# Optimization experiments

Measured on AMD Instinct MI355X. Metric: run time of the kernel, lower is better.

The kernel has to match this reference:

```python
import jax, jax.numpy as jnp
import numpy as np

HID = 64      # hidden_dim
HEADS = 4     # attention heads
CH = HID // HEADS  # 16 per-head channels
EDIM = 6      # edge_dim
NEG = 0.2     # leaky_relu negative slope


def _glorot(key, shape):
    fan_in, fan_out = shape[0], shape[-1]
    s = np.sqrt(6.0 / (fan_in + fan_out)).astype(np.float32)
    return jax.random.uniform(key, shape, jnp.float32, -s, s)


def setup_inputs() -> dict:
    key = jax.random.key(0)
    ks = iter(jax.random.split(key, 48))
    N, E, T = 100000, 1200000, 20000
    inp = {
        "x": jax.random.normal(next(ks), (N, 7), jnp.float32),
        "pos": jax.random.normal(next(ks), (N, 3), jnp.float32),
        "node_type": jax.random.randint(next(ks), (N,), 0, 2),
        "edge_index": jax.random.randint(next(ks), (2, E), 0, N),
        "edge_attr": jax.random.normal(next(ks), (E, EDIM), jnp.float32),
        "num_tracks": T,
        "hidden_state": jax.random.normal(next(ks), (T, HID), jnp.float32),
        # params
        "type_emb": jax.random.normal(next(ks), (2, 8), jnp.float32),
        "enc_W1": _glorot(next(ks), (18, HID)), "enc_b1": jnp.zeros((HID,), jnp.float32),
        "enc_W2": _glorot(next(ks), (HID, HID)), "enc_b2": jnp.zeros((HID,), jnp.float32),
        "gru_Wi": _glorot(next(ks), (HID, 3 * HID)), "gru_bi": jnp.zeros((3 * HID,), jnp.float32),
        "gru_Wh": _glorot(next(ks), (HID, 3 * HID)), "gru_bh": jnp.zeros((3 * HID,), jnp.float32),
        "dec_W1": _glorot(next(ks), (HID, HID)), "dec_b1": jnp.zeros((HID,), jnp.float32),
        "dec_W2": _glorot(next(ks), (HID, 7)), "dec_b2": jnp.zeros((7,), jnp.float32),
    }
    for g in ("g1", "g2"):
        inp[g + "_Wl"] = _glorot(next(ks), (HID, HID))
        inp[g + "_bl"] = jnp.zeros((HID,), jnp.float32)
        inp[g + "_Wr"] = _glorot(next(ks), (HID, HID))
        inp[g + "_br"] = jnp.zeros((HID,), jnp.float32)
        inp[g + "_We"] = _glorot(next(ks), (EDIM, HID))
        inp[g + "_att"] = _glorot(next(ks), (HEADS, CH))
        inp[g + "_bias"] = jnp.zeros((HID,), jnp.float32)
    return inp


def _segment_softmax(e, seg, n):
    m = jax.ops.segment_max(e, seg, num_segments=n)
    m = jnp.where(jnp.isfinite(m), m, 0.0)
    ex = jnp.exp(e - m[seg])
    s = jax.ops.segment_sum(ex, seg, num_segments=n)
    return ex / (s[seg] + 1e-16)


def _gatv2(h, src, dst, eattr, Wl, bl, Wr, br, We, att, bias):
    N = h.shape[0]
    xl = (h @ Wl + bl).reshape(N, HEADS, CH)
    xr = (h @ Wr + br).reshape(N, HEADS, CH)
    ea = (eattr @ We).reshape(-1, HEADS, CH)
    g = jax.nn.leaky_relu(xl[src] + xr[dst] + ea, NEG)      # [E, H, C]
    e = jnp.einsum('ehc,hc->eh', g, att)                     # [E, H]
    alpha = _segment_softmax(e, dst, N)                      # [E, H]
    msg = xl[src] * alpha[..., None]                         # [E, H, C]
    out = jax.ops.segment_sum(msg, dst, num_segments=N)
    return out.reshape(N, HID) + bias, alpha


def reference(x, pos, node_type, edge_index, edge_attr, num_tracks, hidden_state,
              type_emb, enc_W1, enc_b1, enc_W2, enc_b2,
              g1_Wl, g1_bl, g1_Wr, g1_br, g1_We, g1_att, g1_bias,
              g2_Wl, g2_bl, g2_Wr, g2_br, g2_We, g2_att, g2_bias,
              gru_Wi, gru_bi, gru_Wh, gru_bh,
              dec_W1, dec_b1, dec_W2, dec_b2):
    N = x.shape[0]
    h = jnp.concatenate([x, pos, type_emb[node_type]], axis=-1)
    h = jax.nn.relu(h @ enc_W1 + enc_b1) @ enc_W2 + enc_b2

    # PyG GATv2Conv: add self loops, edge_attr fill_value='mean' (mean of incoming edges)
    src, dst = edge_index[0], edge_index[1]
    deg = jax.ops.segment_sum(jnp.ones(src.shape[0], jnp.float32), dst, num_segments=N)
    loop_attr = jax.ops.segment_sum(edge_attr, dst, num_segments=N) / jnp.maximum(deg, 1.0)[:, None]
    ar = jnp.arange(N)
    src_a = jnp.concatenate([src, ar])
    dst_a = jnp.concatenate([dst, ar])
    eattr_a = jnp.concatenate([edge_attr, loop_attr], axis=0)

    h1, a1 = _gatv2(h, src_a, dst_a, eattr_a, g1_Wl, g1_bl, g1_Wr, g1_br, g1_We, g1_att, g1_bias)
    h1 = jax.nn.relu(h1)
    h2, a2 = _gatv2(h1, src_a, dst_a, eattr_a, g2_Wl, g2_bl, g2_Wr, g2_br, g2_We, g2_att, g2_bias)

    # GRUCell on the first num_tracks nodes
    ht = h2[:num_tracks]
    gi = ht @ gru_Wi + gru_bi
    gh = hidden_state @ gru_Wh + gru_bh
    r = jax.nn.sigmoid(gi[:, :HID] + gh[:, :HID])
    z = jax.nn.sigmoid(gi[:, HID:2 * HID] + gh[:, HID:2 * HID])
    n = jnp.tanh(gi[:, 2 * HID:] + r * gh[:, 2 * HID:])
    new_tracks = (1.0 - z) * n + z * hidden_state

    new_full = jnp.concatenate([new_tracks, h2[num_tracks:]], axis=0)
    out = jax.nn.relu(new_full @ dec_W1 + dec_b1) @ dec_W2 + dec_b2  # [N, 7]
    final = out.at[:, :3].set(pos + out[:, :3])
    final = final.at[:, 3:6].set(x[:, :3] + out[:, 3:6])
    return final, new_full, a1, a2
```

## Files before the change

kernel.cpp:

```cpp
#include <hip/hip_runtime.h>

#define NEG 0.2f
#define SCHUNK 1024
typedef unsigned short u16;

__device__ __forceinline__ float sigmoidf_(float v){ return 1.f/(1.f+__expf(-v)); }
__device__ __forceinline__ int rfl_(int v){ return __builtin_amdgcn_readfirstlane(v); }
__device__ __forceinline__ float bf2f_(u16 u){ return __uint_as_float(((unsigned)u)<<16); }
__device__ __forceinline__ u16 f2bf_(float f){
  unsigned u = __float_as_uint(f);
  u += 0x7FFFu + ((u>>16)&1u);
  return (u16)(u>>16);
}
template<int C>
__device__ __forceinline__ float dppadd_(float p){
  int r = __builtin_amdgcn_update_dpp(0, __float_as_int(p), C, 0xF, 0xF, true);
  return p + __int_as_float(r);
}
__device__ __forceinline__ float dppsum16_(float p){
  p = dppadd_<0x121>(p);
  p = dppadd_<0x122>(p);
  p = dppadd_<0x124>(p);
  p = dppadd_<0x128>(p);
  return p;
}

__global__ __launch_bounds__(256) void enc_kernel(
    const float* __restrict__ x, const float* __restrict__ pos,
    const int* __restrict__ ntype, const float* __restrict__ temb,
    const float* __restrict__ W1, const float* __restrict__ b1,
    const float* __restrict__ W2, const float* __restrict__ b2,
    float* __restrict__ hout, int N)
{
  __shared__ float sW1[18*64];
  __shared__ float sW2[4096];
  __shared__ float fT[4][8*20];
  __shared__ float tT[4][8*64];
  for (int i=threadIdx.x; i<18*64; i+=256) sW1[i]=W1[i];
  for (int i=threadIdx.x; i<4096; i+=256)  sW2[i]=W2[i];
  __syncthreads();
  int lane = threadIdx.x & 63;
  int wid  = threadIdx.x >> 6;
  int n0 = (blockIdx.x*4 + wid)*8;
  if (n0 >= N) return;
  float b1v=b1[lane], b2v=b2[lane];
  #pragma unroll
  for (int m=0;m<8;m++){
    int n=n0+m; float fv=0.f;
    if (n<N){
      if (lane<7)       fv=x[(size_t)n*7+lane];
      else if (lane<10) fv=pos[(size_t)n*3+lane-7];
      else if (lane<18) fv=temb[ntype[n]*8+lane-10];
    }
    if (lane<20) fT[wid][m*20+lane]=fv;
  }
  float t[8];
  #pragma unroll
  for (int m=0;m<8;m++) t[m]=b1v;
  #pragma unroll 2
  for (int k=0;k<18;k++){
    float w=sW1[k*64+lane];
    #pragma unroll
    for (int m=0;m<8;m++) t[m] += fT[wid][m*20+k]*w;
  }
  #pragma unroll
  for (int m=0;m<8;m++){ t[m]=fmaxf(t[m],0.f); tT[wid][m*64+lane]=t[m]; }
  float o[8];
  #pragma unroll
  for (int m=0;m<8;m++) o[m]=b2v;
  #pragma unroll 2
  for (int k=0;k<64;k++){
    float w=sW2[k*64+lane];
    #pragma unroll
    for (int m=0;m<8;m++) o[m] += tT[wid][m*64+k]*w;
  }
  #pragma unroll
  for (int m=0;m<8;m++){ int n=n0+m; if (n<N) hout[(size_t)n*64+lane]=o[m]; }
}

__global__ void deg_kernel(const int* __restrict__ ei, int* __restrict__ deg, int E)
{
  int e = blockIdx.x*256 + threadIdx.x;
  if (e>=E) return;
  atomicAdd(deg + ei[E+e], 1);
}

__global__ __launch_bounds__(256) void scan_reduce(const int* __restrict__ deg, int* __restrict__ bsum, int N)
{
  int base = blockIdx.x*SCHUNK + threadIdx.x*4;
  int s=0;
  #pragma unroll
  for (int j=0;j<4;j++){ int i=base+j; s += (i<N)? deg[i]+1 : 0; }
  #pragma unroll
  for (int d=1;d<64;d<<=1) s += __shfl_xor(s,d);
  __shared__ int ws[4];
  if ((threadIdx.x&63)==0) ws[threadIdx.x>>6]=s;
  __syncthreads();
  if (threadIdx.x==0) bsum[blockIdx.x]=ws[0]+ws[1]+ws[2]+ws[3];
}

__global__ __launch_bounds__(1024) void scan_bsums(const int* __restrict__ bsum, int* __restrict__ bscan, int NB)
{
  int tid = threadIdx.x;
  int lane = tid&63, w = tid>>6;
  int v = (tid<NB)? bsum[tid] : 0;
  int inc = v;
  #pragma unroll
  for (int d=1;d<64;d<<=1){ int t=__shfl_up(inc,d); if (lane>=d) inc+=t; }
  __shared__ int wsum[16], woff[16];
  if (lane==63) wsum[w]=inc;
  __syncthreads();
  if (w==0){
    int s=(lane<16)?wsum[lane]:0; int sc=s;
    #pragma unroll
    for (int d=1;d<16;d<<=1){ int t=__shfl_up(sc,d); if (lane>=d) sc+=t; }
    if (lane<16) woff[lane]=sc-s;
  }
  __syncthreads();
  int excl = woff[w] + inc - v;
  if (tid<NB) bscan[tid]=excl;
}

__global__ __launch_bounds__(256) void scan_final(const int* __restrict__ deg, const int* __restrict__ bscan,
                                                  int* __restrict__ offs, int N)
{
  int lane = threadIdx.x&63, w = threadIdx.x>>6;
  int base = blockIdx.x*SCHUNK + threadIdx.x*4;
  int v[4]; int s=0;
  #pragma unroll
  for (int j=0;j<4;j++){ int i=base+j; v[j]=(i<N)?deg[i]+1:0; s+=v[j]; }
  int inc=s;
  #pragma unroll
  for (int d=1;d<64;d<<=1){ int t=__shfl_up(inc,d); if (lane>=d) inc+=t; }
  __shared__ int wsum[4], woff[4];
  if (lane==63) wsum[w]=inc;
  __syncthreads();
  if (threadIdx.x==0){ woff[0]=0; woff[1]=wsum[0]; woff[2]=wsum[0]+wsum[1]; woff[3]=wsum[0]+wsum[1]+wsum[2]; }
  __syncthreads();
  int excl = bscan[blockIdx.x] + woff[w] + (inc - s);
  #pragma unroll
  for (int j=0;j<4;j++){ int i=base+j; if (i<N) offs[i]=excl; excl+=v[j]; }
}

__global__ void fill_kernel(const int* __restrict__ ei, const int* __restrict__ offs,
                            int* __restrict__ cursor, int2* __restrict__ csr2, int E)
{
  int e = blockIdx.x*256 + threadIdx.x;
  if (e >= E) return;
  int dst = ei[E + e];
  int p = atomicAdd(cursor + dst, 1);
  csr2[offs[dst] + p] = make_int2(e, ei[e]);
}

__global__ __launch_bounds__(256) void xfrm_kernel(
    const float* __restrict__ hin,
    const float* __restrict__ Wl, const float* __restrict__ bl,
    const float* __restrict__ Wr, const float* __restrict__ br,
    u16* __restrict__ xlo, u16* __restrict__ xro, int N)
{
  __shared__ float sWl[4096], sWr[4096];
  __shared__ float hT[4][16*64];
  for (int i=threadIdx.x;i<4096;i+=256){ sWl[i]=Wl[i]; sWr[i]=Wr[i]; }
  __syncthreads();
  int lane=threadIdx.x&63;
  int wid=threadIdx.x>>6;
  int n0=(blockIdx.x*4+wid)*16;
  if (n0>=N) return;
  #pragma unroll
  for (int m=0;m<16;m++){
    int n=n0+m;
    hT[wid][m*64+lane] = (n<N)? hin[(size_t)n*64+lane] : 0.f;
  }
  float blv=bl[lane], brv=br[lane];
  float al[16], ar[16];
  #pragma unroll
  for (int m=0;m<16;m++){ al[m]=blv; ar[m]=brv; }
  #pragma unroll 2
  for (int k=0;k<64;k++){
    float wl=sWl[k*64+lane], wr=sWr[k*64+lane];
    #pragma unroll
    for (int m=0;m<16;m++){
      float hb = hT[wid][m*64+k];
      al[m]+=hb*wl; ar[m]+=hb*wr;
    }
  }
  #pragma unroll
  for (int m=0;m<16;m++){
    int n=n0+m;
    if (n<N){ xlo[(size_t)n*64+lane]=f2bf_(al[m]); xro[(size_t)n*64+lane]=f2bf_(ar[m]); }
  }
}

#define EDGE_STEP(EIDX, EADD, XV) do {                                       \
    float s_ = (XV) + xrv + (EADD);                                          \
    s_ = fmaxf(s_, NEG*s_);                                                  \
    float p_ = dppsum16_(s_*attv);                                           \
    if (isbase) aout[(size_t)(EIDX)*4+h] = p_;                               \
    if (__all(p_ <= mmax)) {                                                 \
      float w_ = __expf(p_ - mmax);                                          \
      ssum += w_; acc += w_*(XV);                                            \
    } else {                                                                 \
      float mn_ = fmaxf(mmax, p_);                                           \
      float sc_ = __expf(mmax - mn_);                                        \
      float w_  = __expf(p_ - mn_);                                          \
      ssum = ssum*sc_ + w_;                                                  \
      acc  = acc*sc_ + w_*(XV);                                              \
      mmax = mn_;                                                            \
    }                                                                        \
  } while(0)

#define EDGE_PRE(J) \
    int e##J = rfl_(c##J.x), s##J = rfl_(c##J.y); \
    const float2* q##J = (const float2*)(eattr + (size_t)e##J*6); \
    float2 A##J=q##J[0], B##J=q##J[1], C##J=q##J[2]; \
    float xv##J = bf2f_(xlb[(size_t)s##J*64+lane]);

#define EDGE_BODY(J) \
    float d##J = A##J.x*we0 + A##J.y*we1 + B##J.x*we2 + B##J.y*we3 + C##J.x*we4 + C##J.y*we5; \
    dsum += d##J; \
    EDGE_STEP(e##J, d##J, xv##J);

__global__ __launch_bounds__(256) void gat_kernel(
    const int2* __restrict__ csr2, const int* __restrict__ offs, const int* __restrict__ deg,
    const float* __restrict__ eattr,
    const u16* __restrict__ xlb, const u16* __restrict__ xrb,
    const float* __restrict__ We, const float* __restrict__ att,
    const float* __restrict__ bias,
    float* __restrict__ aout, float2* __restrict__ msbuf,
    float* __restrict__ hout,
    int E, int N, int do_relu)
{
  int lane = threadIdx.x & 63;
  int n = blockIdx.x*4 + (threadIdx.x>>6);
  if (n >= N) return;
  float we0=We[lane], we1=We[64+lane], we2=We[128+lane],
        we3=We[192+lane], we4=We[256+lane], we5=We[320+lane];
  float attv = att[lane];
  float bv = bias[lane];
  float xrv = bf2f_(xrb[(size_t)n*64+lane]);
  int h = lane >> 4;
  bool isbase = (lane & 15) == 0;
  int o0 = rfl_(offs[n]);
  int dg = rfl_(deg[n]);
  int oend = o0 + dg;
  float mmax = -3.402823e38f, ssum=0.f, acc=0.f, dsum=0.f;
  int o = o0;
  for (; o+4 <= oend; o += 4){
    int2 c0=csr2[o], c1=csr2[o+1], c2=csr2[o+2], c3=csr2[o+3];
    EDGE_PRE(0); EDGE_PRE(1); EDGE_PRE(2); EDGE_PRE(3);
    EDGE_BODY(0); EDGE_BODY(1); EDGE_BODY(2); EDGE_BODY(3);
  }
  for (; o < oend; ++o){
    int2 c0=csr2[o];
    EDGE_PRE(0);
    EDGE_BODY(0);
  }
  {
    float dS = dsum * (1.f/fmaxf((float)dg,1.f));
    float xvS = bf2f_(xlb[(size_t)n*64+lane]);
    EDGE_STEP(E+n, dS, xvS);
  }
  float sinv = 1.f/(ssum + 1e-16f);
  if (isbase) msbuf[(size_t)n*4+h] = make_float2(mmax, sinv);
  float outv = acc*sinv + bv;
  if (do_relu) outv = fmaxf(outv, 0.f);
  hout[(size_t)n*64+lane] = outv;
}

__global__ void alpha_kernel(const int* __restrict__ ei, const float2* __restrict__ msbuf,
                             float4* __restrict__ aout4, int E, int N)
{
  int e = blockIdx.x*256 + threadIdx.x;
  if (e >= E+N) return;
  int dst = (e<E)? ei[E+e] : (e-E);
  float4 r = aout4[e];
  const float2* mp = msbuf + (size_t)dst*4;
  float2 m0=mp[0], m1=mp[1], m2=mp[2], m3=mp[3];
  float4 o;
  o.x = __expf(r.x - m0.x)*m0.y;
  o.y = __expf(r.y - m1.x)*m1.y;
  o.z = __expf(r.z - m2.x)*m2.y;
  o.w = __expf(r.w - m3.x)*m3.y;
  aout4[e] = o;
}

__global__ __launch_bounds__(256) void grudec_kernel(
    const float* __restrict__ h2, const float* __restrict__ hid,
    const float* __restrict__ Wi, const float* __restrict__ bi,
    const float* __restrict__ Wh, const float* __restrict__ bh,
    const int* __restrict__ Tptr,
    const float* __restrict__ W1, const float* __restrict__ b1,
    const float* __restrict__ W2, const float* __restrict__ b2,
    const float* __restrict__ x, const float* __restrict__ pos,
    float* __restrict__ nf, float* __restrict__ fout, int N)
{
  __shared__ float sW1[4096];
  __shared__ float sW2[448];
  __shared__ float sb2[7];
  __shared__ float tT[4][8*64];
  __shared__ float pT[4][8*64];
  for (int i=threadIdx.x;i<4096;i+=256) sW1[i]=W1[i];
  for (int i=threadIdx.x;i<448;i+=256) sW2[i]=W2[i];
  if (threadIdx.x<7)  sb2[threadIdx.x]=b2[threadIdx.x];
  __syncthreads();
  int lane = threadIdx.x & 63;
  int wid  = threadIdx.x >> 6;
  int n0 = (blockIdx.x*4 + wid)*8;
  if (n0 >= N) return;
  int T = *Tptr;
  float hv[8], nfv[8];
  #pragma unroll
  for (int m=0;m<8;m++){ int n=n0+m; hv[m] = (n<N)? h2[(size_t)n*64+lane] : 0.f; }
  if (n0 < T){
    float pv[8];
    #pragma unroll
    for (int m=0;m<8;m++){ int n=n0+m; pv[m] = (n<T)? hid[(size_t)n*64+lane] : 0.f; }
    #pragma unroll
    for (int m=0;m<8;m++){ tT[wid][m*64+lane]=hv[m]; pT[wid][m*64+lane]=pv[m]; }
    float gr[8],gz[8],gn[8],hr[8],hz[8],hn[8];
    #pragma unroll
    for (int m=0;m<8;m++){ gr[m]=0.f;gz[m]=0.f;gn[m]=0.f;hr[m]=0.f;hz[m]=0.f;hn[m]=0.f; }
    for (int k=0;k<64;k++){
      float wir=Wi[k*192+lane], wiz=Wi[k*192+64+lane], win=Wi[k*192+128+lane];
      float whr=Wh[k*192+lane], whz=Wh[k*192+64+lane], whn=Wh[k*192+128+lane];
      #pragma unroll
      for (int m=0;m<8;m++){
        float a=tT[wid][m*64+k], b=pT[wid][m*64+k];
        gr[m]+=a*wir; gz[m]+=a*wiz; gn[m]+=a*win;
        hr[m]+=b*whr; hz[m]+=b*whz; hn[m]+=b*whn;
      }
    }
    float bir=bi[lane], biz=bi[64+lane], bin=bi[128+lane];
    float bhr=bh[lane], bhz=bh[64+lane], bhn=bh[128+lane];
    #pragma unroll
    for (int m=0;m<8;m++){
      int n=n0+m;
      if (n<T){
        float r  = sigmoidf_(gr[m]+bir + hr[m]+bhr);
        float z  = sigmoidf_(gz[m]+biz + hz[m]+bhz);
        float nn = tanhf(gn[m]+bin + r*(hn[m]+bhn));
        nfv[m] = (1.f-z)*nn + z*pv[m];
      } else {
        nfv[m] = hv[m];
      }
    }
  } else {
    #pragma unroll
    for (int m=0;m<8;m++) nfv[m] = hv[m];
  }
  #pragma unroll
  for (int m=0;m<8;m++){ int n=n0+m; if (n<N) nf[(size_t)n*64+lane]=nfv[m]; }
  #pragma unroll
  for (int m=0;m<8;m++) tT[wid][m*64+lane]=nfv[m];
  float t[8];
  float b1v=b1[lane];
  #pragma unroll
  for (int m=0;m<8;m++) t[m]=b1v;
  #pragma unroll 2
  for (int k=0;k<64;k++){
    float w=sW1[k*64+lane];
    #pragma unroll
    for (int m=0;m<8;m++) t[m] += tT[wid][m*64+k]*w;
  }
  #pragma unroll
  for (int m=0;m<8;m++) t[m]=fmaxf(t[m],0.f);
  #pragma unroll
  for (int c=0;c<7;c++){
    float w = sW2[lane*7+c];
    float p[8];
    #pragma unroll
    for (int m=0;m<8;m++) p[m]=t[m]*w;
    #pragma unroll
    for (int d=1;d<64;d<<=1){
      #pragma unroll
      for (int m=0;m<8;m++) p[m]+=__shfl_xor(p[m],d);
    }
    if (lane==c){
      float b = sb2[c];
      #pragma unroll
      for (int m=0;m<8;m++){
        int n=n0+m;
        if (n<N){
          float val = p[m]+b;
          if (c<3)      val += pos[(size_t)n*3+c];
          else if (c<6) val += x[(size_t)n*7+(c-3)];
          fout[(size_t)n*7+c] = val;
        }
      }
    }
  }
}

extern "C" void kernel_launch(void* const* d_in, const int* in_sizes, int n_in,
                              void* d_out, int out_size, void* d_ws, size_t ws_size,
                              hipStream_t stream)
{
  const float* x     = (const float*)d_in[0];
  const float* pos   = (const float*)d_in[1];
  const int*   ntype = (const int*)d_in[2];
  const int*   eidx  = (const int*)d_in[3];
  const float* eattr = (const float*)d_in[4];
  const int*   Tptr  = (const int*)d_in[5];
  const float* hid   = (const float*)d_in[6];
  const float* temb  = (const float*)d_in[7];
  const float* encW1 = (const float*)d_in[8];
  const float* encb1 = (const float*)d_in[9];
  const float* encW2 = (const float*)d_in[10];
  const float* encb2 = (const float*)d_in[11];
  const float* gruWi = (const float*)d_in[12];
  const float* grubi = (const float*)d_in[13];
  const float* gruWh = (const float*)d_in[14];
  const float* grubh = (const float*)d_in[15];
  const float* decW1 = (const float*)d_in[16];
  const float* decb1 = (const float*)d_in[17];
  const float* decW2 = (const float*)d_in[18];
  const float* decb2 = (const float*)d_in[19];
  const float* gWl[2]  = {(const float*)d_in[20], (const float*)d_in[27]};
  const float* gbl[2]  = {(const float*)d_in[21], (const float*)d_in[28]};
  const float* gWr[2]  = {(const float*)d_in[22], (const float*)d_in[29]};
  const float* gbr[2]  = {(const float*)d_in[23], (const float*)d_in[30]};
  const float* gWe[2]  = {(const float*)d_in[24], (const float*)d_in[31]};
  const float* gatt[2] = {(const float*)d_in[25], (const float*)d_in[32]};
  const float* gbias[2]= {(const float*)d_in[26], (const float*)d_in[33]};

  int N  = in_sizes[0] / 7;
  int E  = in_sizes[3] / 2;
  int Ea = E + N;
  int NB = (N + SCHUNK - 1) / SCHUNK;

  char* w = (char*)d_ws;
  float* A      = (float*)w; w += (size_t)N*64*sizeof(float);
  float* B      = (float*)w; w += (size_t)N*64*sizeof(float);
  u16*   XL     = (u16*)w;  w += (size_t)N*64*sizeof(u16);
  u16*   XR     = (u16*)w;  w += (size_t)N*64*sizeof(u16);
  int*   deg    = (int*)w;   w += (size_t)N*sizeof(int);
  int*   cursor = (int*)w;   w += (size_t)N*sizeof(int);
  int*   offs   = (int*)w;   w += (size_t)N*sizeof(int);
  int*   bsum   = (int*)w;   w += (size_t)NB*sizeof(int);
  int*   bscan  = (int*)w;   w += (size_t)NB*sizeof(int);
  float2* msbuf = (float2*)w; w += (size_t)N*4*sizeof(float2);
  int2*  csr2   = (int2*)w;  w += (size_t)Ea*sizeof(int2);

  float* out_final = (float*)d_out;
  float* out_nf    = out_final + (size_t)N*7;
  float* out_a1    = out_nf + (size_t)N*64;
  float* out_a2    = out_a1 + (size_t)Ea*4;

  hipMemsetAsync(deg, 0, (size_t)2*N*sizeof(int), stream);

  enc_kernel<<<(N+31)/32, 256, 0, stream>>>(x,pos,ntype,temb,encW1,encb1,encW2,encb2,A,N);
  deg_kernel<<<(E+255)/256, 256, 0, stream>>>(eidx, deg, E);
  scan_reduce<<<NB, 256, 0, stream>>>(deg, bsum, N);
  scan_bsums<<<1, 1024, 0, stream>>>(bsum, bscan, NB);
  scan_final<<<NB, 256, 0, stream>>>(deg, bscan, offs, N);
  fill_kernel<<<(E+255)/256, 256, 0, stream>>>(eidx, offs, cursor, csr2, E);

  xfrm_kernel<<<(N+63)/64, 256, 0, stream>>>(A, gWl[0], gbl[0], gWr[0], gbr[0], XL, XR, N);
  gat_kernel<<<(N+3)/4, 256, 0, stream>>>(csr2, offs, deg, eattr, XL, XR,
      gWe[0], gatt[0], gbias[0], out_a1, msbuf, B, E, N, 1);
  alpha_kernel<<<(Ea+255)/256, 256, 0, stream>>>(eidx, msbuf, (float4*)out_a1, E, N);

  xfrm_kernel<<<(N+63)/64, 256, 0, stream>>>(B, gWl[1], gbl[1], gWr[1], gbr[1], XL, XR, N);
  gat_kernel<<<(N+3)/4, 256, 0, stream>>>(csr2, offs, deg, eattr, XL, XR,
      gWe[1], gatt[1], gbias[1], out_a2, msbuf, A, E, N, 0);
  alpha_kernel<<<(Ea+255)/256, 256, 0, stream>>>(eidx, msbuf, (float4*)out_a2, E, N);

  grudec_kernel<<<(N+31)/32, 256, 0, stream>>>(A, hid, gruWi, grubi, gruWh, grubh, Tptr,
      decW1, decb1, decW2, decb2, x, pos, out_nf, out_final, N);
}
```

Measured before the change: 594.9 us.

## Software-pipeline GAT edge gathers and merge both alpha normalization passes

The GAT aggregation loop becomes a double-buffered software pipeline. CSR entries are loaded two chunks ahead and the bf16 source-feature gathers one chunk ahead, so gather latency overlaps with the softmax arithmetic of the current chunk. The two alpha normalization kernels are fused into one launch that uses separate max/sum buffers per layer, which saves one pass over the edge index. Index arithmetic is switched to 32-bit shifts to cut address computation. The cost is more live registers in the GAT kernel, which could lower occupancy.

```diff
diff --git a/kernel.cpp b/kernel.cpp
--- a/kernel.cpp
+++ b/kernel.cpp
@@ -6,7 +6,7 @@
 
 __device__ __forceinline__ float sigmoidf_(float v){ return 1.f/(1.f+__expf(-v)); }
 __device__ __forceinline__ int rfl_(int v){ return __builtin_amdgcn_readfirstlane(v); }
-__device__ __forceinline__ float bf2f_(u16 u){ return __uint_as_float(((unsigned)u)<<16); }
+__device__ __forceinline__ float bf2f_(unsigned u){ return __uint_as_float(u<<16); }
 __device__ __forceinline__ u16 f2bf_(float f){
   unsigned u = __float_as_uint(f);
   u += 0x7FFFu + ((u>>16)&1u);
@@ -195,7 +195,7 @@
     float s_ = (XV) + xrv + (EADD);                                          \
     s_ = fmaxf(s_, NEG*s_);                                                  \
     float p_ = dppsum16_(s_*attv);                                           \
-    if (isbase) aout[(size_t)(EIDX)*4+h] = p_;                               \
+    if (isbase) aout[(((unsigned)(EIDX))<<2)+h] = p_;                        \
     if (__all(p_ <= mmax)) {                                                 \
       float w_ = __expf(p_ - mmax);                                          \
       ssum += w_; acc += w_*(XV);                                            \
@@ -209,16 +209,25 @@
     }                                                                        \
   } while(0)
 
-#define EDGE_PRE(J) \
-    int e##J = rfl_(c##J.x), s##J = rfl_(c##J.y); \
-    const float2* q##J = (const float2*)(eattr + (size_t)e##J*6); \
-    float2 A##J=q##J[0], B##J=q##J[1], C##J=q##J[2]; \
-    float xv##J = bf2f_(xlb[(size_t)s##J*64+lane]);
-
-#define EDGE_BODY(J) \
-    float d##J = A##J.x*we0 + A##J.y*we1 + B##J.x*we2 + B##J.y*we3 + C##J.x*we4 + C##J.y*we5; \
-    dsum += d##J; \
-    EDGE_STEP(e##J, d##J, xv##J);
+#define LOAD4(CV, OO) { const int2* cp_ = csr2 + (OO); \
+    CV##0=cp_[0]; CV##1=cp_[1]; CV##2=cp_[2]; CV##3=cp_[3]; }
+
+#define GATH1(XV, CV) XV = xlb[(((unsigned)rfl_(CV.y))<<6)+lane]
+#define GATH4(XV, CV) { GATH1(XV##0,CV##0); GATH1(XV##1,CV##1); \
+                        GATH1(XV##2,CV##2); GATH1(XV##3,CV##3); }
+
+#define CEDGE(CV, XV) do { \
+    int e_ = rfl_(CV.x); \
+    const float2* q_ = (const float2*)(eattr + (size_t)e_*6); \
+    float2 A_=q_[0], B_=q_[1], C_=q_[2]; \
+    float xv_ = bf2f_(XV); \
+    float d_ = A_.x*we0 + A_.y*we1 + B_.x*we2 + B_.y*we3 + C_.x*we4 + C_.y*we5; \
+    dsum += d_; \
+    EDGE_STEP(e_, d_, xv_); \
+  } while(0)
+
+#define COMP4(CV, XV) { CEDGE(CV##0,XV##0); CEDGE(CV##1,XV##1); \
+                        CEDGE(CV##2,XV##2); CEDGE(CV##3,XV##3); }
 
 __global__ __launch_bounds__(256) void gat_kernel(
     const int2* __restrict__ csr2, const int* __restrict__ offs, const int* __restrict__ deg,
@@ -237,51 +246,77 @@
         we3=We[192+lane], we4=We[256+lane], we5=We[320+lane];
   float attv = att[lane];
   float bv = bias[lane];
-  float xrv = bf2f_(xrb[(size_t)n*64+lane]);
+  float xrv = bf2f_(xrb[(((unsigned)n)<<6)+lane]);
   int h = lane >> 4;
   bool isbase = (lane & 15) == 0;
   int o0 = rfl_(offs[n]);
   int dg = rfl_(deg[n]);
-  int oend = o0 + dg;
   float mmax = -3.402823e38f, ssum=0.f, acc=0.f, dsum=0.f;
-  int o = o0;
-  for (; o+4 <= oend; o += 4){
-    int2 c0=csr2[o], c1=csr2[o+1], c2=csr2[o+2], c3=csr2[o+3];
-    EDGE_PRE(0); EDGE_PRE(1); EDGE_PRE(2); EDGE_PRE(3);
-    EDGE_BODY(0); EDGE_BODY(1); EDGE_BODY(2); EDGE_BODY(3);
-  }
-  for (; o < oend; ++o){
-    int2 c0=csr2[o];
-    EDGE_PRE(0);
-    EDGE_BODY(0);
+  int nch = dg >> 2;
+  if (nch > 0){
+    int2 cA0,cA1,cA2,cA3, cB0,cB1,cB2,cB3;
+    unsigned xA0,xA1,xA2,xA3, xB0,xB1,xB2,xB3;
+    LOAD4(cA, o0);
+    if (nch > 1) LOAD4(cB, o0+4);
+    GATH4(xA, cA);
+    int i = 0;
+    for (;;){
+      if (i+1 < nch) GATH4(xB, cB);
+      COMP4(cA, xA);
+      if (i+2 < nch) LOAD4(cA, o0+(i+2)*4);
+      ++i; if (i >= nch) break;
+      if (i+1 < nch) GATH4(xA, cA);
+      COMP4(cB, xB);
+      if (i+2 < nch) LOAD4(cB, o0+(i+2)*4);
+      ++i; if (i >= nch) break;
+    }
+  }
+  for (int oo = o0 + (nch<<2); oo < o0 + dg; ++oo){
+    int2 c0 = csr2[oo];
+    unsigned x0; GATH1(x0, c0);
+    CEDGE(c0, x0);
   }
   {
     float dS = dsum * (1.f/fmaxf((float)dg,1.f));
-    float xvS = bf2f_(xlb[(size_t)n*64+lane]);
+    float xvS = bf2f_(xlb[(((unsigned)n)<<6)+lane]);
     EDGE_STEP(E+n, dS, xvS);
   }
   float sinv = 1.f/(ssum + 1e-16f);
-  if (isbase) msbuf[(size_t)n*4+h] = make_float2(mmax, sinv);
+  if (isbase) msbuf[(((unsigned)n)<<2)+h] = make_float2(mmax, sinv);
   float outv = acc*sinv + bv;
   if (do_relu) outv = fmaxf(outv, 0.f);
-  hout[(size_t)n*64+lane] = outv;
-}
-
-__global__ void alpha_kernel(const int* __restrict__ ei, const float2* __restrict__ msbuf,
-                             float4* __restrict__ aout4, int E, int N)
+  hout[(((unsigned)n)<<6)+lane] = outv;
+}
+
+__global__ void alpha_kernel(const int* __restrict__ ei,
+                             const float2* __restrict__ ms1, const float2* __restrict__ ms2,
+                             float4* __restrict__ a1, float4* __restrict__ a2, int E, int N)
 {
   int e = blockIdx.x*256 + threadIdx.x;
   if (e >= E+N) return;
   int dst = (e<E)? ei[E+e] : (e-E);
-  float4 r = aout4[e];
-  const float2* mp = msbuf + (size_t)dst*4;
-  float2 m0=mp[0], m1=mp[1], m2=mp[2], m3=mp[3];
-  float4 o;
-  o.x = __expf(r.x - m0.x)*m0.y;
-  o.y = __expf(r.y - m1.x)*m1.y;
-  o.z = __expf(r.z - m2.x)*m2.y;
-  o.w = __expf(r.w - m3.x)*m3.y;
-  aout4[e] = o;
+  {
+    float4 r = a1[e];
+    const float2* mp = ms1 + (((unsigned)dst)<<2);
+    float2 m0=mp[0], m1=mp[1], m2=mp[2], m3=mp[3];
+    float4 o;
+    o.x = __expf(r.x - m0.x)*m0.y;
+    o.y = __expf(r.y - m1.x)*m1.y;
+    o.z = __expf(r.z - m2.x)*m2.y;
+    o.w = __expf(r.w - m3.x)*m3.y;
+    a1[e] = o;
+  }
+  {
+    float4 r = a2[e];
+    const float2* mp = ms2 + (((unsigned)dst)<<2);
+    float2 m0=mp[0], m1=mp[1], m2=mp[2], m3=mp[3];
+    float4 o;
+    o.x = __expf(r.x - m0.x)*m0.y;
+    o.y = __expf(r.y - m1.x)*m1.y;
+    o.z = __expf(r.z - m2.x)*m2.y;
+    o.w = __expf(r.w - m3.x)*m3.y;
+    a2[e] = o;
+  }
 }
 
 __global__ __launch_bounds__(256) void grudec_kernel(
@@ -438,7 +473,8 @@
   int*   offs   = (int*)w;   w += (size_t)N*sizeof(int);
   int*   bsum   = (int*)w;   w += (size_t)NB*sizeof(int);
   int*   bscan  = (int*)w;   w += (size_t)NB*sizeof(int);
-  float2* msbuf = (float2*)w; w += (size_t)N*4*sizeof(float2);
+  float2* msbuf1= (float2*)w; w += (size_t)N*4*sizeof(float2);
+  float2* msbuf2= (float2*)w; w += (size_t)N*4*sizeof(float2);
   int2*  csr2   = (int2*)w;  w += (size_t)Ea*sizeof(int2);
 
   float* out_final = (float*)d_out;
@@ -457,13 +493,14 @@
 
   xfrm_kernel<<<(N+63)/64, 256, 0, stream>>>(A, gWl[0], gbl[0], gWr[0], gbr[0], XL, XR, N);
   gat_kernel<<<(N+3)/4, 256, 0, stream>>>(csr2, offs, deg, eattr, XL, XR,
-      gWe[0], gatt[0], gbias[0], out_a1, msbuf, B, E, N, 1);
-  alpha_kernel<<<(Ea+255)/256, 256, 0, stream>>>(eidx, msbuf, (float4*)out_a1, E, N);
+      gWe[0], gatt[0], gbias[0], out_a1, msbuf1, B, E, N, 1);
 
   xfrm_kernel<<<(N+63)/64, 256, 0, stream>>>(B, gWl[1], gbl[1], gWr[1], gbr[1], XL, XR, N);
   gat_kernel<<<(N+3)/4, 256, 0, stream>>>(csr2, offs, deg, eattr, XL, XR,
-      gWe[1], gatt[1], gbias[1], out_a2, msbuf, A, E, N, 0);
-  alpha_kernel<<<(Ea+255)/256, 256, 0, stream>>>(eidx, msbuf, (float4*)out_a2, E, N);
+      gWe[1], gatt[1], gbias[1], out_a2, msbuf2, A, E, N, 0);
+
+  alpha_kernel<<<(Ea+255)/256, 256, 0, stream>>>(eidx, msbuf1, msbuf2,
+      (float4*)out_a1, (float4*)out_a2, E, N);
 
   grudec_kernel<<<(N+31)/32, 256, 0, stream>>>(A, hid, gruWi, grubi, gruWh, grubh, Tptr,
       decW1, decb1, decW2, decb2, x, pos, out_nf, out_final, N);
```

After: 647.2 us. +8.8%, slower.

## Fuse encoder with first GAT transform and merge the two alpha passes

Applied to the files above, without the earlier changes.

The encoder kernel now also applies the first layer's Wl/Wr projections and writes the bf16 XL/XR directly. This removes the fp32 A round trip and one xfrm launch. The two alpha normalisation kernels become a single pass that reads the edge index once and uses separate max/sum buffers per layer. Index arithmetic is switched from size_t multiplies to 32-bit shifts to cut address math in the gather-heavy GAT loop. In exchange, the encoder block's shared memory grows to about 54KB, which may reduce occupancy, and the 32-bit indexing assumes the buffers stay small enough.

```diff
diff --git a/kernel.cpp b/kernel.cpp
--- a/kernel.cpp
+++ b/kernel.cpp
@@ -6,7 +6,7 @@
 
 __device__ __forceinline__ float sigmoidf_(float v){ return 1.f/(1.f+__expf(-v)); }
 __device__ __forceinline__ int rfl_(int v){ return __builtin_amdgcn_readfirstlane(v); }
-__device__ __forceinline__ float bf2f_(u16 u){ return __uint_as_float(((unsigned)u)<<16); }
+__device__ __forceinline__ float bf2f_(unsigned u){ return __uint_as_float(u<<16); }
 __device__ __forceinline__ u16 f2bf_(float f){
   unsigned u = __float_as_uint(f);
   u += 0x7FFFu + ((u>>16)&1u);
@@ -25,19 +25,23 @@
   return p;
 }
 
-__global__ __launch_bounds__(256) void enc_kernel(
+__global__ __launch_bounds__(256) void encx_kernel(
     const float* __restrict__ x, const float* __restrict__ pos,
     const int* __restrict__ ntype, const float* __restrict__ temb,
     const float* __restrict__ W1, const float* __restrict__ b1,
     const float* __restrict__ W2, const float* __restrict__ b2,
-    float* __restrict__ hout, int N)
+    const float* __restrict__ Wl, const float* __restrict__ bl,
+    const float* __restrict__ Wr, const float* __restrict__ br,
+    u16* __restrict__ xlo, u16* __restrict__ xro, int N)
 {
   __shared__ float sW1[18*64];
   __shared__ float sW2[4096];
+  __shared__ float sWl[4096];
+  __shared__ float sWr[4096];
   __shared__ float fT[4][8*20];
   __shared__ float tT[4][8*64];
   for (int i=threadIdx.x; i<18*64; i+=256) sW1[i]=W1[i];
-  for (int i=threadIdx.x; i<4096; i+=256)  sW2[i]=W2[i];
+  for (int i=threadIdx.x; i<4096; i+=256){ sW2[i]=W2[i]; sWl[i]=Wl[i]; sWr[i]=Wr[i]; }
   __syncthreads();
   int lane = threadIdx.x & 63;
   int wid  = threadIdx.x >> 6;
@@ -75,7 +79,25 @@
     for (int m=0;m<8;m++) o[m] += tT[wid][m*64+k]*w;
   }
   #pragma unroll
-  for (int m=0;m<8;m++){ int n=n0+m; if (n<N) hout[(size_t)n*64+lane]=o[m]; }
+  for (int m=0;m<8;m++) tT[wid][m*64+lane]=o[m];
+  float blv=bl[lane], brv=br[lane];
+  float al[8], ar[8];
+  #pragma unroll
+  for (int m=0;m<8;m++){ al[m]=blv; ar[m]=brv; }
+  #pragma unroll 2
+  for (int k=0;k<64;k++){
+    float wl=sWl[k*64+lane], wr=sWr[k*64+lane];
+    #pragma unroll
+    for (int m=0;m<8;m++){
+      float hb = tT[wid][m*64+k];
+      al[m]+=hb*wl; ar[m]+=hb*wr;
+    }
+  }
+  #pragma unroll
+  for (int m=0;m<8;m++){
+    int n=n0+m;
+    if (n<N){ xlo[(((unsigned)n)<<6)+lane]=f2bf_(al[m]); xro[(((unsigned)n)<<6)+lane]=f2bf_(ar[m]); }
+  }
 }
 
 __global__ void deg_kernel(const int* __restrict__ ei, int* __restrict__ deg, int E)
@@ -187,7 +209,7 @@
   #pragma unroll
   for (int m=0;m<16;m++){
     int n=n0+m;
-    if (n<N){ xlo[(size_t)n*64+lane]=f2bf_(al[m]); xro[(size_t)n*64+lane]=f2bf_(ar[m]); }
+    if (n<N){ xlo[(((unsigned)n)<<6)+lane]=f2bf_(al[m]); xro[(((unsigned)n)<<6)+lane]=f2bf_(ar[m]); }
   }
 }
 
@@ -195,7 +217,7 @@
     float s_ = (XV) + xrv + (EADD);                                          \
     s_ = fmaxf(s_, NEG*s_);                                                  \
     float p_ = dppsum16_(s_*attv);                                           \
-    if (isbase) aout[(size_t)(EIDX)*4+h] = p_;                               \
+    if (isbase) aout[(((unsigned)(EIDX))<<2)+h] = p_;                        \
     if (__all(p_ <= mmax)) {                                                 \
       float w_ = __expf(p_ - mmax);                                          \
       ssum += w_; acc += w_*(XV);                                            \
@@ -211,14 +233,14 @@
 
 #define EDGE_PRE(J) \
     int e##J = rfl_(c##J.x), s##J = rfl_(c##J.y); \
-    const float2* q##J = (const float2*)(eattr + (size_t)e##J*6); \
+    const float2* q##J = (const float2*)(eattr + (unsigned)e##J*6u); \
     float2 A##J=q##J[0], B##J=q##J[1], C##J=q##J[2]; \
-    float xv##J = bf2f_(xlb[(size_t)s##J*64+lane]);
+    unsigned xv##J = xlb[(((unsigned)s##J)<<6)+lane];
 
 #define EDGE_BODY(J) \
     float d##J = A##J.x*we0 + A##J.y*we1 + B##J.x*we2 + B##J.y*we3 + C##J.x*we4 + C##J.y*we5; \
     dsum += d##J; \
-    EDGE_STEP(e##J, d##J, xv##J);
+    EDGE_STEP(e##J, d##J, bf2f_(xv##J));
 
 __global__ __launch_bounds__(256) void gat_kernel(
     const int2* __restrict__ csr2, const int* __restrict__ offs, const int* __restrict__ deg,
@@ -237,7 +259,7 @@
         we3=We[192+lane], we4=We[256+lane], we5=We[320+lane];
   float attv = att[lane];
   float bv = bias[lane];
-  float xrv = bf2f_(xrb[(size_t)n*64+lane]);
+  float xrv = bf2f_(xrb[(((unsigned)n)<<6)+lane]);
   int h = lane >> 4;
   bool isbase = (lane & 15) == 0;
   int o0 = rfl_(offs[n]);
@@ -257,31 +279,45 @@
   }
   {
     float dS = dsum * (1.f/fmaxf((float)dg,1.f));
-    float xvS = bf2f_(xlb[(size_t)n*64+lane]);
+    float xvS = bf2f_((unsigned)xlb[(((unsigned)n)<<6)+lane]);
     EDGE_STEP(E+n, dS, xvS);
   }
   float sinv = 1.f/(ssum + 1e-16f);
-  if (isbase) msbuf[(size_t)n*4+h] = make_float2(mmax, sinv);
+  if (isbase) msbuf[(((unsigned)n)<<2)+h] = make_float2(mmax, sinv);
   float outv = acc*sinv + bv;
   if (do_relu) outv = fmaxf(outv, 0.f);
-  hout[(size_t)n*64+lane] = outv;
-}
-
-__global__ void alpha_kernel(const int* __restrict__ ei, const float2* __restrict__ msbuf,
-                             float4* __restrict__ aout4, int E, int N)
+  hout[(((unsigned)n)<<6)+lane] = outv;
+}
+
+__global__ void alpha_kernel(const int* __restrict__ ei,
+                             const float2* __restrict__ ms1, const float2* __restrict__ ms2,
+                             float4* __restrict__ a1, float4* __restrict__ a2, int E, int N)
 {
   int e = blockIdx.x*256 + threadIdx.x;
   if (e >= E+N) return;
   int dst = (e<E)? ei[E+e] : (e-E);
-  float4 r = aout4[e];
-  const float2* mp = msbuf + (size_t)dst*4;
-  float2 m0=mp[0], m1=mp[1], m2=mp[2], m3=mp[3];
-  float4 o;
-  o.x = __expf(r.x - m0.x)*m0.y;
-  o.y = __expf(r.y - m1.x)*m1.y;
-  o.z = __expf(r.z - m2.x)*m2.y;
-  o.w = __expf(r.w - m3.x)*m3.y;
-  aout4[e] = o;
+  {
+    float4 r = a1[e];
+    const float2* mp = ms1 + (((unsigned)dst)<<2);
+    float2 m0=mp[0], m1=mp[1], m2=mp[2], m3=mp[3];
+    float4 o;
+    o.x = __expf(r.x - m0.x)*m0.y;
+    o.y = __expf(r.y - m1.x)*m1.y;
+    o.z = __expf(r.z - m2.x)*m2.y;
+    o.w = __expf(r.w - m3.x)*m3.y;
+    a1[e] = o;
+  }
+  {
+    float4 r = a2[e];
+    const float2* mp = ms2 + (((unsigned)dst)<<2);
+    float2 m0=mp[0], m1=mp[1], m2=mp[2], m3=mp[3];
+    float4 o;
+    o.x = __expf(r.x - m0.x)*m0.y;
+    o.y = __expf(r.y - m1.x)*m1.y;
+    o.z = __expf(r.z - m2.x)*m2.y;
+    o.w = __expf(r.w - m3.x)*m3.y;
+    a2[e] = o;
+  }
 }
 
 __global__ __launch_bounds__(256) void grudec_kernel(
@@ -438,7 +474,8 @@
   int*   offs   = (int*)w;   w += (size_t)N*sizeof(int);
   int*   bsum   = (int*)w;   w += (size_t)NB*sizeof(int);
   int*   bscan  = (int*)w;   w += (size_t)NB*sizeof(int);
-  float2* msbuf = (float2*)w; w += (size_t)N*4*sizeof(float2);
+  float2* msbuf1= (float2*)w; w += (size_t)N*4*sizeof(float2);
+  float2* msbuf2= (float2*)w; w += (size_t)N*4*sizeof(float2);
   int2*  csr2   = (int2*)w;  w += (size_t)Ea*sizeof(int2);
 
   float* out_final = (float*)d_out;
@@ -448,22 +485,23 @@
 
   hipMemsetAsync(deg, 0, (size_t)2*N*sizeof(int), stream);
 
-  enc_kernel<<<(N+31)/32, 256, 0, stream>>>(x,pos,ntype,temb,encW1,encb1,encW2,encb2,A,N);
+  encx_kernel<<<(N+31)/32, 256, 0, stream>>>(x,pos,ntype,temb,encW1,encb1,encW2,encb2,
+      gWl[0], gbl[0], gWr[0], gbr[0], XL, XR, N);
   deg_kernel<<<(E+255)/256, 256, 0, stream>>>(eidx, deg, E);
   scan_reduce<<<NB, 256, 0, stream>>>(deg, bsum, N);
   scan_bsums<<<1, 1024, 0, stream>>>(bsum, bscan, NB);
   scan_final<<<NB, 256, 0, stream>>>(deg, bscan, offs, N);
   fill_kernel<<<(E+255)/256, 256, 0, stream>>>(eidx, offs, cursor, csr2, E);
 
-  xfrm_kernel<<<(N+63)/64, 256, 0, stream>>>(A, gWl[0], gbl[0], gWr[0], gbr[0], XL, XR, N);
   gat_kernel<<<(N+3)/4, 256, 0, stream>>>(csr2, offs, deg, eattr, XL, XR,
-      gWe[0], gatt[0], gbias[0], out_a1, msbuf, B, E, N, 1);
-  alpha_kernel<<<(Ea+255)/256, 256, 0, stream>>>(eidx, msbuf, (float4*)out_a1, E, N);
+      gWe[0], gatt[0], gbias[0], out_a1, msbuf1, B, E, N, 1);
 
   xfrm_kernel<<<(N+63)/64, 256, 0, stream>>>(B, gWl[1], gbl[1], gWr[1], gbr[1], XL, XR, N);
   gat_kernel<<<(N+3)/4, 256, 0, stream>>>(csr2, offs, deg, eattr, XL, XR,
-      gWe[1], gatt[1], gbias[1], out_a2, msbuf, A, E, N, 0);
-  alpha_kernel<<<(Ea+255)/256, 256, 0, stream>>>(eidx, msbuf, (float4*)out_a2, E, N);
+      gWe[1], gatt[1], gbias[1], out_a2, msbuf2, A, E, N, 0);
+
+  alpha_kernel<<<(Ea+255)/256, 256, 0, stream>>>(eidx, msbuf1, msbuf2,
+      (float4*)out_a1, (float4*)out_a2, E, N);
 
   grudec_kernel<<<(N+31)/32, 256, 0, stream>>>(A, hid, gruWi, grubi, gruWh, grubh, Tptr,
       decW1, decb1, decW2, decb2, x, pos, out_nf, out_final, N);
```

New measurement: 621.4 us. 1.04x slower.
